# Performance work log

Measured on AMD Instinct MI355X. Metric: run time of the kernel, lower is better.

The kernel has to match this reference:

```python
import jax, jax.numpy as jnp
import numpy as np

EPS = 1e-5
NUM_HEADS = 8
BLOCK_SIZE = 8


def _ln(x, w, b):
    mu = jnp.mean(x, axis=-1, keepdims=True)
    var = jnp.mean((x - mu) ** 2, axis=-1, keepdims=True)
    return (x - mu) * jax.lax.rsqrt(var + EPS) * w + b


def _mha(x, wqkv, bqkv, wo, bo, allowed):
    # x: [b,t,d]; wqkv: [3d,d]; allowed: [t,t] bool (True = attend)
    b, t, d = x.shape
    h, hd = NUM_HEADS, d // NUM_HEADS
    qkv = x @ wqkv.T + bqkv
    q, k, v = jnp.split(qkv, 3, axis=-1)
    q = q.reshape(b, t, h, hd)
    k = k.reshape(b, t, h, hd)
    v = v.reshape(b, t, h, hd)
    scores = jnp.einsum('bihd,bjhd->bhij', q, k) / np.sqrt(hd).astype(x.dtype)
    scores = jnp.where(allowed[None, None], scores, -jnp.inf)
    attn = jax.nn.softmax(scores, axis=-1)
    out = jnp.einsum('bhij,bjhd->bihd', attn, v).reshape(b, t, d)
    return out @ wo.T + bo


def setup_inputs() -> dict:
    key = jax.random.key(0)
    ks = jax.random.split(key, 20)
    B, T, D, FF, L, MAXT = 64, 512, 256, 512, 4, 512
    s = 0.02
    return {
        'latents': jax.random.normal(ks[0], (B, T, D), dtype=jnp.float32),
        'move_ids': jax.random.randint(ks[1], (B, T), 0, 20480),
        'mask': jax.random.randint(ks[2], (B, T), 0, 2).astype(bool),
        'positional': s * jax.random.normal(ks[3], (1, MAXT, D), dtype=jnp.float32),
        'embed_from': s * jax.random.normal(ks[4], (64, D), dtype=jnp.float32),
        'embed_to': s * jax.random.normal(ks[5], (64, D), dtype=jnp.float32),
        'embed_promo': s * jax.random.normal(ks[6], (5, D), dtype=jnp.float32),
        'in_proj_w': s * jax.random.normal(ks[7], (L, 3 * D, D), dtype=jnp.float32),
        'in_proj_b': jnp.zeros((L, 3 * D), dtype=jnp.float32),
        'out_w': s * jax.random.normal(ks[8], (L, D, D), dtype=jnp.float32),
        'out_b': jnp.zeros((L, D), dtype=jnp.float32),
        'fc1_w': s * jax.random.normal(ks[9], (L, FF, D), dtype=jnp.float32),
        'fc1_b': jnp.zeros((L, FF), dtype=jnp.float32),
        'fc2_w': s * jax.random.normal(ks[10], (L, D, FF), dtype=jnp.float32),
        'fc2_b': jnp.zeros((L, D), dtype=jnp.float32),
        'norm_w': jnp.ones((D,), dtype=jnp.float32),
        'norm_b': jnp.zeros((D,), dtype=jnp.float32),
    }


def reference(latents, move_ids, mask, positional, embed_from, embed_to,
              embed_promo, in_proj_w, in_proj_b, out_w, out_b,
              fc1_w, fc1_b, fc2_w, fc2_b, norm_w, norm_b):
    b, t, d = latents.shape
    # move-id decomposition: promo/from/to embedding sum
    promo = move_ids // 4096
    rem = move_ids % 4096
    frm = rem // 64
    to = rem % 64
    x = latents + positional[:, :t, :] + embed_from[frm] + embed_to[to] + embed_promo[promo]
    # block-causal mask: token i may attend j iff block(j) <= block(i)
    bidx = jnp.arange(t) // BLOCK_SIZE
    allowed = bidx[None, :] <= bidx[:, None]
    n_layers = in_proj_w.shape[0]
    for l in range(n_layers):
        # NOTE: the single LayerNorm (norm_w, norm_b) is shared everywhere,
        # exactly as in the original module.
        x = x + _mha(_ln(x, norm_w, norm_b), in_proj_w[l], in_proj_b[l],
                     out_w[l], out_b[l], allowed)
        h1 = jax.nn.relu(_ln(x, norm_w, norm_b) @ fc1_w[l].T + fc1_b[l])
        x = x + h1 @ fc2_w[l].T + fc2_b[l]
    x = _ln(x, norm_w, norm_b)
    return jnp.where(mask[..., None], x, latents)
```

## Files before the change

kernel.cpp:

```cpp
#include <hip/hip_runtime.h>
#include <math.h>

#define Bv  64
#define Tv  512
#define Dv  256
#define FFv 512
#define Lv  4
#define BTv (Bv*Tv)
#define EPSv 1e-5f
#define QSC 0.25509402f

typedef __attribute__((ext_vector_type(8))) short short8;
typedef __attribute__((ext_vector_type(4))) float f32x4;
typedef unsigned short us;

#if __has_builtin(__builtin_amdgcn_exp2f)
#define EXP2(x) __builtin_amdgcn_exp2f(x)
#else
#define EXP2(x) exp2f(x)
#endif

__device__ __forceinline__ us f2bf(float f) {
    unsigned r;
    asm("v_cvt_pk_bf16_f32 %0, %1, 0" : "=v"(r) : "v"(f));
    return (us)r;
}
__device__ __forceinline__ unsigned pk2(float a, float b) {
    unsigned r;
    asm("v_cvt_pk_bf16_f32 %0, %1, %2" : "=v"(r) : "v"(a), "v"(b));
    return r;
}
__device__ __forceinline__ float wave_sum(float v) {
#pragma unroll
    for (int o = 32; o > 0; o >>= 1) v += __shfl_xor(v, o);
    return v;
}

__global__ __launch_bounds__(256) void cvtall_kernel(
    const float* __restrict__ qw, const float* __restrict__ ow,
    const float* __restrict__ f1, const float* __restrict__ f2,
    const float* __restrict__ qb,
    us* __restrict__ wq, us* __restrict__ wo, us* __restrict__ w1,
    us* __restrict__ w2, float* __restrict__ sb)
{
    int blk = blockIdx.x, tid = threadIdx.x;
    if (blk < 2048) {
        const float* s; us* d; int i; float sc = 1.0f;
        if (blk < 768)       { i = blk*256 + tid;        s = qw; d = wq;
                               sc = (((i >> 6) % 768) < 256) ? QSC : 1.0f; }
        else if (blk < 1024) { i = (blk-768)*256 + tid;  s = ow; d = wo; }
        else if (blk < 1536) { i = (blk-1024)*256 + tid; s = f1; d = w1; }
        else                 { i = (blk-1536)*256 + tid; s = f2; d = w2; }
        float4 v = ((const float4*)s)[i];
        uint2 o;
        o.x = pk2(v.x*sc, v.y*sc);
        o.y = pk2(v.z*sc, v.w*sc);
        ((uint2*)d)[i] = o;
    } else {
        int i = (blk-2048)*256 + tid;
        sb[i] = qb[i] * (((i % 768) < 256) ? QSC : 1.0f);
    }
}

__global__ __launch_bounds__(256) void embed_ln_kernel(
    const float* __restrict__ lat, const int* __restrict__ mids,
    const float* __restrict__ pos, const float* __restrict__ ef,
    const float* __restrict__ et,  const float* __restrict__ ep,
    const float* __restrict__ nw,  const float* __restrict__ nb,
    float* __restrict__ x, us* __restrict__ xn)
{
    int wv = threadIdx.x >> 6, lane = threadIdx.x & 63;
    size_t row = (size_t)blockIdx.x * 4 + wv;
    int t  = (int)(row & (Tv - 1));
    int id = mids[row];
    int promo = id >> 12;
    int rem   = id & 4095;
    int frm   = rem >> 6;
    int to    = rem & 63;
    float4 v  = ((const float4*)(lat + row*Dv))[lane];
    float4 pv = ((const float4*)(pos + (size_t)t*Dv))[lane];
    float4 fv = ((const float4*)(ef + (size_t)frm*Dv))[lane];
    float4 tv = ((const float4*)(et + (size_t)to*Dv))[lane];
    float4 ev = ((const float4*)(ep + (size_t)promo*Dv))[lane];
    v.x += pv.x + fv.x + tv.x + ev.x;
    v.y += pv.y + fv.y + tv.y + ev.y;
    v.z += pv.z + fv.z + tv.z + ev.z;
    v.w += pv.w + fv.w + tv.w + ev.w;
    ((float4*)(x + row*Dv))[lane] = v;
    float mu = wave_sum(v.x + v.y + v.z + v.w) * (1.0f/Dv);
    float dx = v.x-mu, dy = v.y-mu, dz = v.z-mu, dw = v.w-mu;
    float var = wave_sum(dx*dx + dy*dy + dz*dz + dw*dw) * (1.0f/Dv);
    float inv = rsqrtf(var + EPSv);
    float4 w4 = ((const float4*)nw)[lane];
    float4 b4 = ((const float4*)nb)[lane];
    uint2 o;
    o.x = pk2(dx*inv*w4.x + b4.x, dy*inv*w4.y + b4.y);
    o.y = pk2(dz*inv*w4.z + b4.z, dw*inv*w4.w + b4.w);
    ((uint2*)(xn + row*Dv))[lane] = o;
}

__global__ __launch_bounds__(256) void final_kernel(
    const float* __restrict__ x, const float* __restrict__ lat,
    const int* __restrict__ mask, const float* __restrict__ w,
    const float* __restrict__ b, float* __restrict__ out)
{
    int wv = threadIdx.x >> 6, lane = threadIdx.x & 63;
    size_t row = (size_t)blockIdx.x * 4 + wv;
    float4 v = ((const float4*)(x + row*Dv))[lane];
    float mu = wave_sum(v.x + v.y + v.z + v.w) * (1.0f/Dv);
    float dx = v.x-mu, dy = v.y-mu, dz = v.z-mu, dw = v.w-mu;
    float var = wave_sum(dx*dx + dy*dy + dz*dz + dw*dw) * (1.0f/Dv);
    float inv = rsqrtf(var + EPSv);
    float4 w4 = ((const float4*)w)[lane];
    float4 b4 = ((const float4*)b)[lane];
    float4 o;
    o.x = dx*inv*w4.x + b4.x;
    o.y = dy*inv*w4.y + b4.y;
    o.z = dz*inv*w4.z + b4.z;
    o.w = dw*inv*w4.w + b4.w;
    if (!mask[row]) o = ((const float4*)(lat + row*Dv))[lane];
    ((float4*)(out + row*Dv))[lane] = o;
}

template<int RELU>
__global__ __launch_bounds__(256) void mm_kernel(
    const us* __restrict__ A, const us* __restrict__ B,
    const float* __restrict__ bias, us* __restrict__ C,
    int M, int N, int K)
{
    __shared__ us As[128*64];
    __shared__ us Bs[128*64];
    int tid  = threadIdx.x;
    int lane = tid & 63;
    int wu   = __builtin_amdgcn_readfirstlane(tid >> 6);
    int m0 = blockIdx.x * 128, n0 = blockIdx.y * 128;
    int wm = wu & 1, wn = wu >> 1;
    f32x4 acc[4][4] = {};
    int srow = lane >> 3;
    int sg   = (lane & 7) ^ srow;
    const us* Ag = A + (size_t)m0 * K + sg*8;
    const us* Bg = B + (size_t)n0 * K + sg*8;
    int cc = lane & 15, q4 = lane >> 4;
    for (int k0 = 0; k0 < K; k0 += 64) {
        __syncthreads();
#pragma unroll
        for (int p = 0; p < 4; p++) {
            int row = wu*32 + p*8;
            __builtin_amdgcn_global_load_lds(
                (const __attribute__((address_space(1))) unsigned int*)(Ag + (size_t)(row + srow)*K + k0),
                (__attribute__((address_space(3))) unsigned int*)(As + row*64),
                16, 0, 0);
            __builtin_amdgcn_global_load_lds(
                (const __attribute__((address_space(1))) unsigned int*)(Bg + (size_t)(row + srow)*K + k0),
                (__attribute__((address_space(3))) unsigned int*)(Bs + row*64),
                16, 0, 0);
        }
        __syncthreads();
#pragma unroll
        for (int h = 0; h < 2; h++) {
            int pg = ((h*4 + q4) ^ (cc & 7)) * 8;
            short8 av[4], bv[4];
#pragma unroll
            for (int i = 0; i < 4; i++)
                av[i] = *(const short8*)(As + (wm*64 + i*16 + cc)*64 + pg);
#pragma unroll
            for (int j = 0; j < 4; j++)
                bv[j] = *(const short8*)(Bs + (wn*64 + j*16 + cc)*64 + pg);
#pragma unroll
            for (int i = 0; i < 4; i++)
#pragma unroll
                for (int j = 0; j < 4; j++)
                    acc[i][j] = __builtin_amdgcn_mfma_f32_16x16x32_bf16(av[i], bv[j], acc[i][j], 0, 0, 0);
        }
    }
#pragma unroll
    for (int j = 0; j < 4; j++) {
        int n = n0 + wn*64 + j*16 + cc;
        float bj = bias[n];
#pragma unroll
        for (int i = 0; i < 4; i++) {
#pragma unroll
            for (int r = 0; r < 4; r++) {
                int m = m0 + wm*64 + i*16 + q4*4 + r;
                float v = acc[i][j][r] + bj;
                if (RELU) v = fmaxf(v, 0.f);
                C[(size_t)m * N + n] = f2bf(v);
            }
        }
    }
}

__global__ __launch_bounds__(256) void mm256_kernel(
    const us* __restrict__ A, const us* __restrict__ B,
    const float* __restrict__ bias, float* __restrict__ x,
    us* __restrict__ xn, const float* __restrict__ nw,
    const float* __restrict__ nb, int M, int K)
{
    __shared__ us As[64*64];
    __shared__ us Bs[256*64];
    __shared__ float red[64][4][2];
    __shared__ float mus[64], rss[64];
    int tid  = threadIdx.x;
    int lane = tid & 63;
    int wu   = __builtin_amdgcn_readfirstlane(tid >> 6);
    int m0 = blockIdx.x * 64;
    f32x4 acc[4][4] = {};
    int srow = lane >> 3;
    int sg   = (lane & 7) ^ srow;
    const us* Ag = A + (size_t)m0 * K + sg*8;
    const us* Bg = B + sg*8;
    int cc = lane & 15, q4 = lane >> 4;
    for (int k0 = 0; k0 < K; k0 += 64) {
        __syncthreads();
#pragma unroll
        for (int p = 0; p < 2; p++) {
            int row = wu*16 + p*8;
            __builtin_amdgcn_global_load_lds(
                (const __attribute__((address_space(1))) unsigned int*)(Ag + (size_t)(row + srow)*K + k0),
                (__attribute__((address_space(3))) unsigned int*)(As + row*64),
                16, 0, 0);
        }
#pragma unroll
        for (int p = 0; p < 8; p++) {
            int row = wu*64 + p*8;
            __builtin_amdgcn_global_load_lds(
                (const __attribute__((address_space(1))) unsigned int*)(Bg + (size_t)(row + srow)*K + k0),
                (__attribute__((address_space(3))) unsigned int*)(Bs + row*64),
                16, 0, 0);
        }
        __syncthreads();
#pragma unroll
        for (int h = 0; h < 2; h++) {
            int pg = ((h*4 + q4) ^ (cc & 7)) * 8;
            short8 av[4], bv[4];
#pragma unroll
            for (int i = 0; i < 4; i++)
                av[i] = *(const short8*)(As + (i*16 + cc)*64 + pg);
#pragma unroll
            for (int j = 0; j < 4; j++)
                bv[j] = *(const short8*)(Bs + (wu*64 + j*16 + cc)*64 + pg);
#pragma unroll
            for (int i = 0; i < 4; i++)
#pragma unroll
                for (int j = 0; j < 4; j++)
                    acc[i][j] = __builtin_amdgcn_mfma_f32_16x16x32_bf16(av[i], bv[j], acc[i][j], 0, 0, 0);
        }
    }
    float bb[4], nwv[4], nbv[4];
#pragma unroll
    for (int j = 0; j < 4; j++) {
        int n = wu*64 + j*16 + cc;
        bb[j] = bias[n]; nwv[j] = nw[n]; nbv[j] = nb[n];
    }
#pragma unroll
    for (int i = 0; i < 4; i++) {
        float s[4] = {0.f,0.f,0.f,0.f}, sq[4] = {0.f,0.f,0.f,0.f};
#pragma unroll
        for (int j = 0; j < 4; j++) {
#pragma unroll
            for (int r = 0; r < 4; r++) {
                int m = m0 + i*16 + q4*4 + r;
                size_t off = (size_t)m * Dv + wu*64 + j*16 + cc;
                float v = acc[i][j][r] + bb[j] + x[off];
                acc[i][j][r] = v;
                x[off] = v;
                s[r] += v; sq[r] += v*v;
            }
        }
#pragma unroll
        for (int r = 0; r < 4; r++) {
#pragma unroll
            for (int o = 1; o < 16; o <<= 1) {
                s[r]  += __shfl_xor(s[r],  o);
                sq[r] += __shfl_xor(sq[r], o);
            }
        }
        if (cc == 0) {
#pragma unroll
            for (int r = 0; r < 4; r++) {
                red[i*16 + q4*4 + r][wu][0] = s[r];
                red[i*16 + q4*4 + r][wu][1] = sq[r];
            }
        }
    }
    __syncthreads();
    if (tid < 64) {
        float ts = red[tid][0][0] + red[tid][1][0] + red[tid][2][0] + red[tid][3][0];
        float tq = red[tid][0][1] + red[tid][1][1] + red[tid][2][1] + red[tid][3][1];
        float mu = ts * (1.0f/Dv);
        float var = tq * (1.0f/Dv) - mu*mu;
        mus[tid] = mu;
        rss[tid] = rsqrtf(var + EPSv);
    }
    __syncthreads();
#pragma unroll
    for (int i = 0; i < 4; i++) {
#pragma unroll
        for (int r = 0; r < 4; r++) {
            int ml = i*16 + q4*4 + r;
            float mu = mus[ml], rv = rss[ml];
#pragma unroll
            for (int j = 0; j < 4; j++) {
                size_t off = (size_t)(m0 + ml) * Dv + wu*64 + j*16 + cc;
                xn[off] = f2bf((acc[i][j][r] - mu)*rv*nwv[j] + nbv[j]);
            }
        }
    }
}

__global__ __launch_bounds__(256) void attn_kernel(
    const us* __restrict__ qkv, us* __restrict__ ao)
{
    int blk = blockIdx.x;
    int b  = blk & 63;
    int h  = (blk >> 6) & 7;
    int qt = blk >> 9;
    int i0 = qt << 6;
    int tid = threadIdx.x;
    int lane = tid & 63;
    int wu = tid >> 6;

    __shared__ us Ks[2][64][40];
    __shared__ us Vt[2][32][72];
    __shared__ us Ps[4][16][72];
    __shared__ float Ls[4][16];

    size_t rowbase = (size_t)b * Tv;
    int c = lane & 15, q4 = lane >> 4;

    short8 qfrag = *(const short8*)(qkv + (rowbase + i0 + wu*16 + c)*768 + h*32 + q4*8);

    int skey = tid >> 2, sdc = (tid & 3) << 3;
    int vkey = tid & 63, vg = tid >> 6;
    const us* kgp = qkv + (rowbase + skey)*768 + 256 + h*32 + sdc;
    const us* vgp = qkv + (rowbase + vkey)*768 + 512 + h*32 + vg*8;

    f32x4 oacc[2] = {};
    float lsum = 0.f;
    int ntiles = qt + 1;

    short8 kreg = *(const short8*)(kgp);
    short8 vreg = *(const short8*)(vgp);
    *(short8*)&Ks[0][skey][sdc] = kreg;
#pragma unroll
    for (int j = 0; j < 8; j++) Vt[0][vg*8 + j][vkey] = vreg[j];
    if (ntiles > 1) {
        kreg = *(const short8*)(kgp + 64*768);
        vreg = *(const short8*)(vgp + 64*768);
    }
    __syncthreads();

    for (int kt = 0; kt < ntiles; kt++) {
        int cur = kt & 1;
        if (kt + 1 < ntiles) {
            *(short8*)&Ks[cur^1][skey][sdc] = kreg;
#pragma unroll
            for (int j = 0; j < 8; j++) Vt[cur^1][vg*8 + j][vkey] = vreg[j];
        }
        if (kt + 2 < ntiles) {
            kreg = *(const short8*)(kgp + (size_t)(kt+2)*64*768);
            vreg = *(const short8*)(vgp + (size_t)(kt+2)*64*768);
        }

        f32x4 st[4];
#pragma unroll
        for (int jt = 0; jt < 4; jt++) {
            short8 kf = *(const short8*)&Ks[cur][jt*16 + c][q4*8];
            st[jt] = __builtin_amdgcn_mfma_f32_16x16x32_bf16(kf, qfrag, (f32x4){0.f,0.f,0.f,0.f}, 0, 0, 0);
        }
        bool diag = (kt == ntiles - 1);
#pragma unroll
        for (int jt = 0; jt < 4; jt++) {
            float msk = (!diag || (2*jt + (q4 >> 1) <= 2*wu + (c >> 3))) ? 1.f : 0.f;
            float p0 = EXP2(st[jt][0]) * msk;
            float p1 = EXP2(st[jt][1]) * msk;
            float p2 = EXP2(st[jt][2]) * msk;
            float p3 = EXP2(st[jt][3]) * msk;
            lsum += p0 + p1 + p2 + p3;
            uint2 w2; w2.x = pk2(p0, p1); w2.y = pk2(p2, p3);
            *(uint2*)&Ps[wu][c][jt*16 + q4*4] = w2;
        }
#pragma unroll
        for (int kk = 0; kk < 2; kk++) {
            short8 pf = *(const short8*)&Ps[wu][c][kk*32 + q4*8];
#pragma unroll
            for (int dt = 0; dt < 2; dt++) {
                short8 vf = *(const short8*)&Vt[cur][dt*16 + c][kk*32 + q4*8];
                oacc[dt] = __builtin_amdgcn_mfma_f32_16x16x32_bf16(pf, vf, oacc[dt], 0, 0, 0);
            }
        }
        __syncthreads();
    }

    float l = lsum;
    l += __shfl_xor(l, 16);
    l += __shfl_xor(l, 32);
    if (q4 == 0) Ls[wu][c] = 1.0f / l;
    float4 lv4 = *(const float4*)&Ls[wu][q4*4];
#pragma unroll
    for (int dt = 0; dt < 2; dt++) {
#pragma unroll
        for (int r = 0; r < 4; r++) {
            float li = (r == 0) ? lv4.x : (r == 1) ? lv4.y : (r == 2) ? lv4.z : lv4.w;
            ao[(rowbase + i0 + wu*16 + q4*4 + r)*256 + h*32 + dt*16 + c] = f2bf(oacc[dt][r] * li);
        }
    }
}

extern "C" void kernel_launch(void* const* d_in, const int* in_sizes, int n_in,
                              void* d_out, int out_size, void* d_ws, size_t ws_size,
                              hipStream_t stream)
{
    const float* latents    = (const float*)d_in[0];
    const int*   move_ids   = (const int*)  d_in[1];
    const int*   mask       = (const int*)  d_in[2];
    const float* positional = (const float*)d_in[3];
    const float* embed_from = (const float*)d_in[4];
    const float* embed_to   = (const float*)d_in[5];
    const float* embed_promo= (const float*)d_in[6];
    const float* in_proj_w  = (const float*)d_in[7];
    const float* in_proj_b  = (const float*)d_in[8];
    const float* out_w      = (const float*)d_in[9];
    const float* out_b      = (const float*)d_in[10];
    const float* fc1_w      = (const float*)d_in[11];
    const float* fc1_b      = (const float*)d_in[12];
    const float* fc2_w      = (const float*)d_in[13];
    const float* fc2_b      = (const float*)d_in[14];
    const float* norm_w     = (const float*)d_in[15];
    const float* norm_b     = (const float*)d_in[16];
    float* out = (float*)d_out;

    float* x   = (float*)d_ws;
    float* sb  = x + (size_t)BTv * Dv;
    us* xn  = (us*)(sb + Lv*768);
    us* qkv = xn + (size_t)BTv * Dv;
    us* ao  = qkv + (size_t)BTv * 768;
    us* h1  = ao + (size_t)BTv * Dv;
    us* wq  = h1 + (size_t)BTv * FFv;
    us* wo  = wq + (size_t)Lv * 768 * Dv;
    us* w1  = wo + (size_t)Lv * Dv * Dv;
    us* w2  = w1 + (size_t)Lv * FFv * Dv;

    cvtall_kernel<<<2060, 256, 0, stream>>>(in_proj_w, out_w, fc1_w, fc2_w,
                                            in_proj_b, wq, wo, w1, w2, sb);

    embed_ln_kernel<<<BTv/4, 256, 0, stream>>>(latents, move_ids, positional,
        embed_from, embed_to, embed_promo, norm_w, norm_b, x, xn);

    for (int l = 0; l < Lv; l++) {
        mm_kernel<0><<<dim3(BTv/128, 768/128), 256, 0, stream>>>(
            xn, wq + (size_t)l*768*Dv, sb + l*768, qkv, BTv, 768, Dv);
        attn_kernel<<<Bv*8*(Tv/64), 256, 0, stream>>>(qkv, ao);
        mm256_kernel<<<BTv/64, 256, 0, stream>>>(
            ao, wo + (size_t)l*Dv*Dv, out_b + l*Dv, x, xn, norm_w, norm_b,
            BTv, Dv);
        mm_kernel<1><<<dim3(BTv/128, FFv/128), 256, 0, stream>>>(
            xn, w1 + (size_t)l*FFv*Dv, fc1_b + l*FFv, h1, BTv, FFv, Dv);
        mm256_kernel<<<BTv/64, 256, 0, stream>>>(
            h1, w2 + (size_t)l*Dv*FFv, fc2_b + l*Dv, x, xn, norm_w, norm_b,
            BTv, FFv);
    }
    final_kernel<<<BTv/4, 256, 0, stream>>>(x, latents, mask, norm_w, norm_b, out);
}
```

Before: 628.7 us.

## Enlarge QKV/FC1 GEMM tiles to 256x256 with double-buffered LDS staging

Replaces the 128x128 bf16 MFMA GEMM used for the QKV and FC1 projections with a 256x256-tile kernel. It runs 512 threads per block, each wave holding an 8x4 grid of 16x16 accumulators. The K loop now double-buffers LDS and issues the next tile's global-to-LDS loads before computing the current one, with a single barrier per iteration. The goal is more operand reuse per loaded byte and overlapping memory traffic with MFMA work. In exchange, the 128 KB of LDS limits each CU to one block, and the grid shrinks to 256–384 blocks. With K=256 there are only four K iterations, so the overlap gain is limited.

```diff
diff --git a/kernel.cpp b/kernel.cpp
--- a/kernel.cpp
+++ b/kernel.cpp
@@ -123,65 +123,76 @@
 }
 
 template<int RELU>
-__global__ __launch_bounds__(256) void mm_kernel(
+__global__ __launch_bounds__(512, 2) void mm256sq_kernel(
     const us* __restrict__ A, const us* __restrict__ B,
     const float* __restrict__ bias, us* __restrict__ C,
     int M, int N, int K)
 {
-    __shared__ us As[128*64];
-    __shared__ us Bs[128*64];
+    __shared__ us As[2][256*64];
+    __shared__ us Bs[2][256*64];
     int tid  = threadIdx.x;
     int lane = tid & 63;
     int wu   = __builtin_amdgcn_readfirstlane(tid >> 6);
-    int m0 = blockIdx.x * 128, n0 = blockIdx.y * 128;
+    int m0 = blockIdx.x * 256, n0 = blockIdx.y * 256;
     int wm = wu & 1, wn = wu >> 1;
-    f32x4 acc[4][4] = {};
+    f32x4 acc[8][4] = {};
     int srow = lane >> 3;
     int sg   = (lane & 7) ^ srow;
     const us* Ag = A + (size_t)m0 * K + sg*8;
     const us* Bg = B + (size_t)n0 * K + sg*8;
     int cc = lane & 15, q4 = lane >> 4;
-    for (int k0 = 0; k0 < K; k0 += 64) {
-        __syncthreads();
-#pragma unroll
-        for (int p = 0; p < 4; p++) {
-            int row = wu*32 + p*8;
-            __builtin_amdgcn_global_load_lds(
-                (const __attribute__((address_space(1))) unsigned int*)(Ag + (size_t)(row + srow)*K + k0),
-                (__attribute__((address_space(3))) unsigned int*)(As + row*64),
-                16, 0, 0);
-            __builtin_amdgcn_global_load_lds(
-                (const __attribute__((address_space(1))) unsigned int*)(Bg + (size_t)(row + srow)*K + k0),
-                (__attribute__((address_space(3))) unsigned int*)(Bs + row*64),
-                16, 0, 0);
-        }
-        __syncthreads();
+
+#define STG(kk, bb) { \
+    _Pragma("unroll") \
+    for (int p = 0; p < 4; p++) { \
+        int row = wu*32 + p*8; \
+        __builtin_amdgcn_global_load_lds( \
+            (const __attribute__((address_space(1))) unsigned int*)(Ag + (size_t)(row + srow)*K + (kk)), \
+            (__attribute__((address_space(3))) unsigned int*)(&As[bb][row*64]), \
+            16, 0, 0); \
+        __builtin_amdgcn_global_load_lds( \
+            (const __attribute__((address_space(1))) unsigned int*)(Bg + (size_t)(row + srow)*K + (kk)), \
+            (__attribute__((address_space(3))) unsigned int*)(&Bs[bb][row*64]), \
+            16, 0, 0); \
+    } }
+
+    STG(0, 0);
+    __syncthreads();
+    int nk = K >> 6;
+    int cur = 0;
+    for (int t = 0; t < nk; t++) {
+        if (t + 1 < nk) {
+            if (cur) STG((t+1)*64, 0) else STG((t+1)*64, 1)
+        }
 #pragma unroll
         for (int h = 0; h < 2; h++) {
             int pg = ((h*4 + q4) ^ (cc & 7)) * 8;
-            short8 av[4], bv[4];
-#pragma unroll
-            for (int i = 0; i < 4; i++)
-                av[i] = *(const short8*)(As + (wm*64 + i*16 + cc)*64 + pg);
+            short8 av[8], bv[4];
+#pragma unroll
+            for (int i = 0; i < 8; i++)
+                av[i] = *(const short8*)(&As[cur][(wm*128 + i*16 + cc)*64 + pg]);
 #pragma unroll
             for (int j = 0; j < 4; j++)
-                bv[j] = *(const short8*)(Bs + (wn*64 + j*16 + cc)*64 + pg);
-#pragma unroll
-            for (int i = 0; i < 4; i++)
+                bv[j] = *(const short8*)(&Bs[cur][(wn*64 + j*16 + cc)*64 + pg]);
+#pragma unroll
+            for (int i = 0; i < 8; i++)
 #pragma unroll
                 for (int j = 0; j < 4; j++)
                     acc[i][j] = __builtin_amdgcn_mfma_f32_16x16x32_bf16(av[i], bv[j], acc[i][j], 0, 0, 0);
         }
-    }
+        __syncthreads();
+        cur ^= 1;
+    }
+#undef STG
 #pragma unroll
     for (int j = 0; j < 4; j++) {
         int n = n0 + wn*64 + j*16 + cc;
         float bj = bias[n];
 #pragma unroll
-        for (int i = 0; i < 4; i++) {
+        for (int i = 0; i < 8; i++) {
 #pragma unroll
             for (int r = 0; r < 4; r++) {
-                int m = m0 + wm*64 + i*16 + q4*4 + r;
+                int m = m0 + wm*128 + i*16 + q4*4 + r;
                 float v = acc[i][j][r] + bj;
                 if (RELU) v = fmaxf(v, 0.f);
                 C[(size_t)m * N + n] = f2bf(v);
@@ -448,13 +459,13 @@
         embed_from, embed_to, embed_promo, norm_w, norm_b, x, xn);
 
     for (int l = 0; l < Lv; l++) {
-        mm_kernel<0><<<dim3(BTv/128, 768/128), 256, 0, stream>>>(
+        mm256sq_kernel<0><<<dim3(BTv/256, 768/256), 512, 0, stream>>>(
             xn, wq + (size_t)l*768*Dv, sb + l*768, qkv, BTv, 768, Dv);
         attn_kernel<<<Bv*8*(Tv/64), 256, 0, stream>>>(qkv, ao);
         mm256_kernel<<<BTv/64, 256, 0, stream>>>(
             ao, wo + (size_t)l*Dv*Dv, out_b + l*Dv, x, xn, norm_w, norm_b,
             BTv, Dv);
-        mm_kernel<1><<<dim3(BTv/128, FFv/128), 256, 0, stream>>>(
+        mm256sq_kernel<1><<<dim3(BTv/256, FFv/256), 512, 0, stream>>>(
             xn, w1 + (size_t)l*FFv*Dv, fc1_b + l*FFv, h1, BTv, FFv, Dv);
         mm256_kernel<<<BTv/64, 256, 0, stream>>>(
             h1, w2 + (size_t)l*Dv*FFv, fc2_b + l*Dv, x, xn, norm_w, norm_b,
```

After: 638.0 us. About the same (+1.5%).
